# Kernel optimization log

Hardware: AMD Instinct MI355X
Metric: run time of the kernel (lower is better)

The kernel has to match this reference:

```python
import jax, jax.numpy as jnp
import numpy as np

EMBED_DIM = 1024
NUM_HEADS = 16
HEAD_DIM = EMBED_DIM // NUM_HEADS
SCALING = HEAD_DIM ** -0.5
T, B = 1024, 4


def setup_inputs() -> dict:
    key = jax.random.key(0)
    k1, k2, k3, k4 = jax.random.split(key, 4)
    x_TBC = jax.random.normal(k1, (T, B, EMBED_DIM), dtype=jnp.float32)
    key_padding_mask = jnp.zeros((B, T), dtype=bool)
    edge_bias = jax.random.normal(k2, (B, NUM_HEADS, T, T), dtype=jnp.float32)
    # xavier_uniform-ish init for weights
    lim_qkv = (6.0 / (EMBED_DIM + 3 * EMBED_DIM)) ** 0.5 / (2 ** 0.5)
    w_qkv = jax.random.uniform(k3, (3 * EMBED_DIM, EMBED_DIM), minval=-lim_qkv, maxval=lim_qkv, dtype=jnp.float32)
    b_qkv = jnp.zeros((3 * EMBED_DIM,), dtype=jnp.float32)
    lim_p = (6.0 / (2 * EMBED_DIM)) ** 0.5
    w_proj = jax.random.uniform(k4, (EMBED_DIM, EMBED_DIM), minval=-lim_p, maxval=lim_p, dtype=jnp.float32)
    b_proj = jnp.zeros((EMBED_DIM,), dtype=jnp.float32)
    return {"x_TBC": x_TBC, "key_padding_mask": key_padding_mask, "edge_bias": edge_bias,
            "w_qkv": w_qkv, "b_qkv": b_qkv, "w_proj": w_proj, "b_proj": b_proj}


def reference(x_TBC, key_padding_mask, edge_bias, w_qkv, b_qkv, w_proj, b_proj):
    Tn, Bn, C = x_TBC.shape
    H, Dh = NUM_HEADS, HEAD_DIM
    qkv = x_TBC @ w_qkv.T + b_qkv               # [T,B,3C]
    q, k, v = jnp.split(qkv, 3, axis=-1)
    def split_heads(t):  # [T,B,C] -> [B,H,T,Dh]
        return t.reshape(Tn, Bn, H, Dh).transpose(1, 2, 0, 3)
    q = split_heads(q) * SCALING
    k = split_heads(k)
    v = split_heads(v)
    logits = jnp.einsum('bhtd,bhsd->bhts', q, k) + edge_bias  # [B,H,T,T]
    neg_inf = jnp.finfo(logits.dtype).min
    logits = jnp.where(key_padding_mask[:, None, None, :], neg_inf, logits)
    attn = jax.nn.softmax(logits, axis=-1)
    out = jnp.einsum('bhts,bhsd->bhtd', attn, v)  # [B,H,T,Dh]
    out = out.transpose(2, 0, 1, 3).reshape(Tn, Bn, C)  # [T,B,C]
    out = out @ w_proj.T + b_proj
    return out
```

## Files before the change

kernel.cpp:

```cpp
#include <hip/hip_runtime.h>
#include <stdint.h>
#include <math.h>

#define TT  1024
#define BBN 4
#define CCH 1024
#define HHN 16
#define DHD 64
#define MMR 4096
#define N3  3072

typedef __attribute__((ext_vector_type(4))) float  f32x4;
typedef __attribute__((ext_vector_type(8))) short  s16x8;
typedef __attribute__((ext_vector_type(8))) __bf16 bf16x8;

static __device__ __forceinline__ f32x4 mfma16(s16x8 a, s16x8 b, f32x4 c) {
  return __builtin_amdgcn_mfma_f32_16x16x32_bf16(
      __builtin_bit_cast(bf16x8, a), __builtin_bit_cast(bf16x8, b), c, 0, 0, 0);
}

static __device__ __forceinline__ unsigned short f2bf(float f) {
  union { float f; unsigned int u; } v; v.f = f;
  unsigned int u = v.u;
  return (unsigned short)((u + 0x7FFFu + ((u >> 16) & 1u)) >> 16);
}

typedef const __attribute__((address_space(1))) void GVoid;
typedef __attribute__((address_space(3))) void LVoid;
static __device__ __forceinline__ void gll16(const void* g, void* l) {
  __builtin_amdgcn_global_load_lds((GVoid*)g, (LVoid*)l, 16, 0, 0);
}

#if __has_builtin(__builtin_amdgcn_exp2f)
#define EXP2F(x) __builtin_amdgcn_exp2f(x)
#else
#define EXP2F(x) exp2f(x)
#endif

__global__ void cvt_all(const float* __restrict__ x, const float* __restrict__ wqkv,
                        const float* __restrict__ wproj, unsigned short* __restrict__ out) {
  int i = blockIdx.x * blockDim.x + threadIdx.x;
  const float4* src;
  int off;
  if (i < 1048576)      { src = (const float4*)x;     off = 0; }
  else if (i < 1835008) { src = (const float4*)wqkv;  off = 1048576; }
  else                  { src = (const float4*)wproj; off = 1835008; }
  float4 f = src[i - off];
  ushort4 o;
  o.x = f2bf(f.x); o.y = f2bf(f.y); o.z = f2bf(f.z); o.w = f2bf(f.w);
  ((ushort4*)out)[i] = o;
}

__global__ __launch_bounds__(512, 2) void gemm_qkv(
    const unsigned short* __restrict__ A, const unsigned short* __restrict__ Bw,
    const float* __restrict__ bias,
    unsigned short* __restrict__ qb, unsigned short* __restrict__ kb,
    unsigned short* __restrict__ vtb) {
  constexpr int K = 1024;
  constexpr int AH = 256 * 32;
  constexpr int BH = 256 * 32;
  __shared__ __align__(16) unsigned short sMem[3 * AH + 3 * BH];
  unsigned short* sA0 = sMem;
  unsigned short* sB0 = sMem + 3 * AH;
  const int tid = threadIdx.x;
  const int l = tid & 63, w = tid >> 6;
  const int g = l >> 4, c = l & 15;
  const int wr = w >> 2, wc = w & 3;
  const int total = gridDim.x * gridDim.y;
  const int flat = blockIdx.y * gridDim.x + blockIdx.x;
  const int wg = (flat & 7) * (total >> 3) + (flat >> 3);
  const int bxs = wg % gridDim.x, bys = wg / gridDim.x;
  const int bm = bys * 256, bn = bxs * 256;

  const int srow = tid >> 2;
  const int schG = (tid & 3) ^ ((tid >> 3) & 3);
  const unsigned short* Agp = A + (size_t)(bm + srow) * K + schG * 8;
  const unsigned short* Bgp = Bw + (size_t)(bn + srow) * K + schG * 8;
  const int swzR = (c >> 1) & 3;

  f32x4 acc[8][4] = {};

#define QSTAGE(s, h) do {                                                        \
    _Pragma("unroll")                                                            \
    for (int i_ = 0; i_ < 2; ++i_)                                               \
      gll16(Agp + (size_t)(i_ * 128) * K + (s) * 32,                             \
            sA0 + (h) * AH + i_ * 4096 + w * 512);                               \
    _Pragma("unroll")                                                            \
    for (int i_ = 0; i_ < 2; ++i_)                                               \
      gll16(Bgp + (size_t)(i_ * 128) * K + (s) * 32,                             \
            sB0 + (h) * BH + i_ * 4096 + w * 512);                               \
  } while (0)

  const int NS = K >> 5;
  QSTAGE(0, 0);
  QSTAGE(1, 1);
  QSTAGE(2, 2);
  asm volatile("s_waitcnt vmcnt(8)" ::: "memory");
  __builtin_amdgcn_s_barrier();

  int h = 0;
#pragma unroll 1
  for (int s = 0;; ++s) {
    s16x8 af[8], bfr[4];
#pragma unroll
    for (int mi = 0; mi < 8; ++mi)
      af[mi] = *(const s16x8*)&sA0[h * AH + (wr * 128 + mi * 16 + c) * 32 + (g ^ swzR) * 8];
#pragma unroll
    for (int ni = 0; ni < 4; ++ni)
      bfr[ni] = *(const s16x8*)&sB0[h * BH + (wc * 64 + ni * 16 + c) * 32 + (g ^ swzR) * 8];
#pragma unroll
    for (int mi = 0; mi < 8; ++mi)
#pragma unroll
      for (int ni = 0; ni < 4; ++ni)
        acc[mi][ni] = mfma16(af[mi], bfr[ni], acc[mi][ni]);
    if (s == NS - 1) break;
    __builtin_amdgcn_s_barrier();
    if (s + 3 < NS)      { QSTAGE(s + 3, h);
                           asm volatile("s_waitcnt vmcnt(8)" ::: "memory"); }
    else if (s + 2 < NS) { asm volatile("s_waitcnt vmcnt(4)" ::: "memory"); }
    else                 { asm volatile("s_waitcnt vmcnt(0)" ::: "memory"); }
    __builtin_amdgcn_s_barrier();
    h = (h == 2) ? 0 : h + 1;
  }

#undef QSTAGE

  const int part = bn >> 10;
  if (part != 2) {
    const bool isq = (part == 0);
    const float qscale = 0.18033688f;
#pragma unroll
    for (int mi = 0; mi < 8; ++mi)
#pragma unroll
      for (int ni = 0; ni < 4; ++ni) {
        const int col = bn + wc * 64 + ni * 16 + c;
        const float bsv = bias[col];
        const int rem = col & 1023;
        const int hh = rem >> 6, d = rem & 63;
#pragma unroll
        for (int j = 0; j < 4; ++j) {
          const int r = bm + wr * 128 + mi * 16 + g * 4 + j;
          const int t = r >> 2, bb = r & 3;
          const int bh = bb * 16 + hh;
          float av = acc[mi][ni][j] + bsv;
          if (isq) qb[((size_t)bh * 1024 + t) * 64 + d] = f2bf(av * qscale);
          else     kb[((size_t)bh * 1024 + t) * 64 + d] = f2bf(av);
        }
      }
    return;
  }

  unsigned short* sT = sMem;
  const int tl0 = bm >> 2;
  const int bb = w & 3, th = w >> 2;
#pragma unroll 1
  for (int pc = 0; pc < 4; ++pc) {
    __syncthreads();
    if (wc == pc) {
#pragma unroll
      for (int mi = 0; mi < 8; ++mi)
#pragma unroll
        for (int ni = 0; ni < 4; ++ni) {
          const int col = bn + pc * 64 + ni * 16 + c;
          const float bsv = bias[col];
#pragma unroll
          for (int j = 0; j < 4; ++j)
            sT[(wr * 128 + mi * 16 + g * 4 + j) * 72 + ni * 16 + c] =
                f2bf(acc[mi][ni][j] + bsv);
        }
    }
    __syncthreads();
    const int h2 = ((bn + pc * 64) & 1023) >> 6;
    unsigned short* vdst = vtb + ((size_t)(bb * 16 + h2) * 64 + l) * 1024 + tl0 + th * 32;
#pragma unroll
    for (int q8 = 0; q8 < 4; ++q8) {
      unsigned short pk[8];
#pragma unroll
      for (int e = 0; e < 8; ++e)
        pk[e] = sT[(((th * 32 + q8 * 8 + e) << 2) | bb) * 72 + l];
      *(s16x8*)&vdst[q8 * 8] = *(const s16x8*)pk;
    }
  }
}

template <int MODE, int BN>
__global__ __launch_bounds__(256, 4) void gemm_bt(
    const unsigned short* __restrict__ A, const unsigned short* __restrict__ Bw,
    const float* __restrict__ bias, float* __restrict__ Cout, int M, int N, int K) {
  constexpr int NI = BN / 32;
  constexpr int AH = 128 * 32;
  constexpr int BH = BN * 32;
  __shared__ __align__(16) unsigned short sMem[3 * AH + 3 * BH];
  unsigned short* sA0 = sMem;
  unsigned short* sB0 = sMem + 3 * AH;
  const int tid = threadIdx.x;
  const int l = tid & 63, w = tid >> 6;
  const int g = l >> 4, c = l & 15;
  const int wr = w >> 1, wc = w & 1;
  const int total = gridDim.x * gridDim.y;
  const int flat = blockIdx.y * gridDim.x + blockIdx.x;
  const int wg = (flat & 7) * (total >> 3) + (flat >> 3);
  const int bxs = wg % gridDim.x, bys = wg / gridDim.x;
  const int bm = bys * 128, bn = bxs * BN;

  const int srow = w * 16 + (l >> 2);
  const int schG = (l & 3) ^ ((l >> 3) & 3);
  const unsigned short* Agp = A + (size_t)(bm + srow) * K + schG * 8;
  const unsigned short* Bgp = Bw + (size_t)(bn + srow) * K + schG * 8;
  const int swzR = (c >> 1) & 3;

  f32x4 acc[4][NI] = {};

#define GSTAGE(s, h) do {                                                        \
    _Pragma("unroll")                                                            \
    for (int i_ = 0; i_ < 2; ++i_)                                               \
      gll16(Agp + (size_t)(i_ * 64) * K + (s) * 32,                              \
            sA0 + (h) * AH + i_ * 2048 + w * 512);                               \
    _Pragma("unroll")                                                            \
    for (int i_ = 0; i_ < BN / 64; ++i_)                                         \
      gll16(Bgp + (size_t)(i_ * 64) * K + (s) * 32,                              \
            sB0 + (h) * BH + i_ * 2048 + w * 512);                               \
  } while (0)

  const int NS = K >> 5;
  GSTAGE(0, 0);
  GSTAGE(1, 1);
  GSTAGE(2, 2);
  asm volatile("s_waitcnt vmcnt(6)" ::: "memory");
  __builtin_amdgcn_s_barrier();

  int h = 0;
#pragma unroll 1
  for (int s = 0;; ++s) {
    s16x8 af[4], bfr[NI];
#pragma unroll
    for (int mi = 0; mi < 4; ++mi)
      af[mi] = *(const s16x8*)&sA0[h * AH + (wr * 64 + mi * 16 + c) * 32 + (g ^ swzR) * 8];
#pragma unroll
    for (int ni = 0; ni < NI; ++ni)
      bfr[ni] = *(const s16x8*)&sB0[h * BH + (wc * (BN / 2) + ni * 16 + c) * 32 + (g ^ swzR) * 8];
#pragma unroll
    for (int mi = 0; mi < 4; ++mi)
#pragma unroll
      for (int ni = 0; ni < NI; ++ni)
        acc[mi][ni] = mfma16(af[mi], bfr[ni], acc[mi][ni]);
    if (s == NS - 1) break;
    __builtin_amdgcn_s_barrier();
    if (s + 3 < NS)      { GSTAGE(s + 3, h);
                           asm volatile("s_waitcnt vmcnt(6)" ::: "memory"); }
    else if (s + 2 < NS) { asm volatile("s_waitcnt vmcnt(3)" ::: "memory"); }
    else                 { asm volatile("s_waitcnt vmcnt(0)" ::: "memory"); }
    __builtin_amdgcn_s_barrier();
    h = (h == 2) ? 0 : h + 1;
  }

#undef GSTAGE

#pragma unroll
  for (int mi = 0; mi < 4; ++mi)
#pragma unroll
    for (int ni = 0; ni < NI; ++ni) {
      const int col = bn + wc * (BN / 2) + ni * 16 + c;
      const float bsv = bias[col];
#pragma unroll
      for (int j = 0; j < 4; ++j) {
        const int r = bm + wr * 64 + mi * 16 + g * 4 + j;
        Cout[(size_t)r * N + col] = acc[mi][ni][j] + bsv;
      }
    }
}

__global__ __launch_bounds__(256, 3) void attn_kernel(
    const unsigned short* __restrict__ qb, const unsigned short* __restrict__ kb,
    const unsigned short* __restrict__ vtb, const float* __restrict__ eb,
    const unsigned char* __restrict__ mask, unsigned short* __restrict__ ob) {
  __shared__ __align__(16) unsigned short sQ[64 * 64];
  __shared__ __align__(16) unsigned short sK[2][64 * 64];
  __shared__ __align__(16) unsigned short sV[2][64 * 64];
  __shared__ __align__(16) unsigned short sP[4][16 * 72];
  __shared__ __align__(4) unsigned char sM[1024];
  const int tid = threadIdx.x;
  const int l = tid & 63, w = tid >> 6;
  const int g = l >> 4, c = l & 15;
  const int flat = blockIdx.y * 16 + blockIdx.x;
  const int wg = (flat & 7) * 128 + (flat >> 3);
  const int q0 = (wg & 15) * 64;
  const int bh = wg >> 4;
  const int b = bh >> 4;
  const int srow = tid >> 3, sch = tid & 7;

  const unsigned short* qg = qb + (size_t)bh * 65536;
  const unsigned short* kg = kb + (size_t)bh * 65536;
  const unsigned short* vg = vtb + (size_t)bh * 65536;
  const float* ebg = eb + (size_t)bh * 1048576 + (size_t)(q0 + w * 16 + g * 4) * 1024;

  const float BS = 1.44269504f;
  float bvA[4][4], bvB[4][4];
  float ps[4] = {0.f, 0.f, 0.f, 0.f};
  f32x4 po[4] = {};

#define STAGE(tv, P) do {                                                        \
    _Pragma("unroll")                                                            \
    for (int i_ = 0; i_ < 2; ++i_) {                                             \
      int row_ = i_ * 32 + srow;                                                 \
      gll16(kg + (size_t)((tv) * 64 + row_) * 64 + (sch ^ (row_ & 7)) * 8,       \
            &sK[P][i_ * 2048 + w * 512]);                                        \
      gll16(vg + (size_t)row_ * 1024 + (tv) * 64 + (sch ^ (row_ & 7)) * 8,       \
            &sV[P][i_ * 2048 + w * 512]);                                        \
    } } while (0)

#define BIAS(tv, BV) do {                                                        \
    _Pragma("unroll")                                                            \
    for (int ni_ = 0; ni_ < 4; ++ni_)                                            \
      _Pragma("unroll")                                                          \
      for (int j_ = 0; j_ < 4; ++j_)                                             \
        BV[ni_][j_] = ebg[(size_t)j_ * 1024 + (tv) * 64 + ni_ * 16 + c];         \
    } while (0)

#define TILE(P, BV, s0v) do {                                                    \
    float mkc_[4];                                                               \
    _Pragma("unroll")                                                            \
    for (int ni_ = 0; ni_ < 4; ++ni_)                                            \
      mkc_[ni_] = sM[(s0v) + ni_ * 16 + c] ? -1e30f : -8.0f;                     \
    s16x8 kf_[4][2];                                                             \
    _Pragma("unroll")                                                            \
    for (int ni_ = 0; ni_ < 4; ++ni_)                                            \
      _Pragma("unroll")                                                          \
      for (int k2_ = 0; k2_ < 2; ++k2_) {                                        \
        int row_ = ni_ * 16 + c;                                                 \
        kf_[ni_][k2_] = *(const s16x8*)&sK[P][row_ * 64 +                        \
                         (((k2_ * 4 + g) ^ (row_ & 7)) * 8)];                    \
      }                                                                          \
    f32x4 sc_[4] = {};                                                           \
    _Pragma("unroll")                                                            \
    for (int k2_ = 0; k2_ < 2; ++k2_)                                            \
      _Pragma("unroll")                                                          \
      for (int ni_ = 0; ni_ < 4; ++ni_)                                          \
        sc_[ni_] = mfma16(qf[k2_], kf_[ni_][k2_], sc_[ni_]);                     \
    _Pragma("unroll")                                                            \
    for (int ni_ = 0; ni_ < 4; ++ni_)                                            \
      _Pragma("unroll")                                                          \
      for (int j_ = 0; j_ < 4; ++j_) {                                           \
        float x_ = fmaf(BV[ni_][j_], BS, sc_[ni_][j_]) + mkc_[ni_];              \
        float p_ = EXP2F(x_);                                                    \
        sP[w][(g * 4 + j_) * 72 + ni_ * 16 + c] = f2bf(p_);                      \
        ps[j_] += p_;                                                            \
      }                                                                          \
    s16x8 vf_[4][2];                                                             \
    _Pragma("unroll")                                                            \
    for (int nd_ = 0; nd_ < 4; ++nd_)                                            \
      _Pragma("unroll")                                                          \
      for (int k2_ = 0; k2_ < 2; ++k2_) {                                        \
        int row_ = nd_ * 16 + c;                                                 \
        vf_[nd_][k2_] = *(const s16x8*)&sV[P][row_ * 64 +                        \
                         (((k2_ * 4 + g) ^ (row_ & 7)) * 8)];                    \
      }                                                                          \
    asm volatile("s_waitcnt lgkmcnt(0)" ::: "memory");                           \
    __builtin_amdgcn_sched_barrier(0);                                           \
    s16x8 pf_[2];                                                                \
    _Pragma("unroll")                                                            \
    for (int k2_ = 0; k2_ < 2; ++k2_)                                            \
      pf_[k2_] = *(const s16x8*)&sP[w][c * 72 + k2_ * 32 + g * 8];               \
    _Pragma("unroll")                                                            \
    for (int k2_ = 0; k2_ < 2; ++k2_)                                            \
      _Pragma("unroll")                                                          \
      for (int nd_ = 0; nd_ < 4; ++nd_)                                          \
        po[nd_] = mfma16(pf_[k2_], vf_[nd_][k2_], po[nd_]);                      \
  } while (0)

#pragma unroll
  for (int i = 0; i < 2; ++i) {
    int row = i * 32 + srow;
    gll16(qg + (size_t)(q0 + row) * 64 + (sch ^ (row & 7)) * 8, &sQ[i * 2048 + w * 512]);
  }
  STAGE(0, 0);
  STAGE(1, 1);
  BIAS(0, bvA);
  BIAS(1, bvB);
  ((unsigned int*)sM)[tid] = ((const unsigned int*)(mask + b * TT))[tid & 255];
  __syncthreads();

  s16x8 qf[2];
#pragma unroll
  for (int kk2 = 0; kk2 < 2; ++kk2) {
    int row = w * 16 + c;
    qf[kk2] = *(const s16x8*)&sQ[row * 64 + (((kk2 * 4 + g) ^ (row & 7)) * 8)];
  }

#pragma unroll 1
  for (int t2 = 0;; t2 += 2) {
    TILE(0, bvA, t2 * 64);
    __builtin_amdgcn_s_barrier();
    if (t2 + 2 < 16) { STAGE(t2 + 2, 0); BIAS(t2 + 2, bvA); }
    if (t2 == 14) { asm volatile("s_waitcnt vmcnt(16)" ::: "memory"); }
    else          { asm volatile("s_waitcnt vmcnt(36)" ::: "memory"); }
    __builtin_amdgcn_s_barrier();
    TILE(1, bvB, t2 * 64 + 64);
    if (t2 == 14) break;
    __builtin_amdgcn_s_barrier();
    STAGE(t2 + 3, 1); BIAS(t2 + 3, bvB);
    asm volatile("s_waitcnt vmcnt(36)" ::: "memory");
    __builtin_amdgcn_s_barrier();
  }

#undef STAGE
#undef BIAS
#undef TILE

#pragma unroll
  for (int j = 0; j < 4; ++j) {
#pragma unroll
    for (int off = 1; off <= 8; off <<= 1)
      ps[j] += __shfl_xor(ps[j], off, 64);
    ps[j] = 1.0f / ps[j];
  }
  const int h = bh & 15;
#pragma unroll
  for (int nd = 0; nd < 4; ++nd)
#pragma unroll
    for (int j = 0; j < 4; ++j) {
      float val = po[nd][j] * ps[j];
      int t = q0 + w * 16 + g * 4 + j;
      ob[((size_t)t * 4 + b) * 1024 + h * 64 + nd * 16 + c] = f2bf(val);
    }
}

extern "C" void kernel_launch(void* const* d_in, const int* in_sizes, int n_in,
                              void* d_out, int out_size, void* d_ws, size_t ws_size,
                              hipStream_t stream) {
  const float* x      = (const float*)d_in[0];
  const unsigned char* mask = (const unsigned char*)d_in[1];
  const float* ebias  = (const float*)d_in[2];
  const float* wqkv   = (const float*)d_in[3];
  const float* bqkv   = (const float*)d_in[4];
  const float* wproj  = (const float*)d_in[5];
  const float* bproj  = (const float*)d_in[6];
  float* out = (float*)d_out;

  char* ws = (char*)d_ws;
  unsigned short* xb    = (unsigned short*)(ws);
  unsigned short* wqkvb = (unsigned short*)(ws + 8388608);
  unsigned short* wpb   = (unsigned short*)(ws + 14680064);
  unsigned short* qbuf  = (unsigned short*)(ws + 16777216);
  unsigned short* kbuf  = (unsigned short*)(ws + 25165824);
  unsigned short* vtbuf = (unsigned short*)(ws + 33554432);
  unsigned short* obuf  = (unsigned short*)(ws + 41943040);

  cvt_all<<<8192, 256, 0, stream>>>(x, wqkv, wproj, xb);

  gemm_qkv<<<dim3(12, 16), 512, 0, stream>>>(
      xb, wqkvb, bqkv, qbuf, kbuf, vtbuf);

  attn_kernel<<<dim3(16, 64), 256, 0, stream>>>(
      qbuf, kbuf, vtbuf, ebias, mask, obuf);

  gemm_bt<0, 64><<<dim3(16, 32), 256, 0, stream>>>(
      obuf, wpb, bproj, out, MMR, 1024, 1024);
}
```

Before: 157.5 us.

## Restructure QKV GEMM main loop into interleaved load/MFMA double-buffered pipeline

Replaces the 3-stage 32-wide K pipeline in the QKV projection GEMM with a 2-tile-deep scheme of 64-wide K tiles split into halves, using 4 LDS planes per operand. Global-to-LDS loads for the next tile are issued between LDS fragment reads and MFMA groups, and s_setprio raises wave priority around the MFMA bursts. The A fragments are read in halves to cut register pressure, and explicit lgkmcnt waits with sched_barriers fix the ordering. LDS use grows from 6 to 8 planes, which may affect the two-blocks-per-CU occupancy target.

```diff
diff --git a/kernel.cpp b/kernel.cpp
--- a/kernel.cpp
+++ b/kernel.cpp
@@ -57,11 +57,10 @@
     unsigned short* __restrict__ qb, unsigned short* __restrict__ kb,
     unsigned short* __restrict__ vtb) {
   constexpr int K = 1024;
-  constexpr int AH = 256 * 32;
-  constexpr int BH = 256 * 32;
-  __shared__ __align__(16) unsigned short sMem[3 * AH + 3 * BH];
+  constexpr int PH = 256 * 32;
+  __shared__ __align__(16) unsigned short sMem[8 * PH];
   unsigned short* sA0 = sMem;
-  unsigned short* sB0 = sMem + 3 * AH;
+  unsigned short* sB0 = sMem + 4 * PH;
   const int tid = threadIdx.x;
   const int l = tid & 63, w = tid >> 6;
   const int g = l >> 4, c = l & 15;
@@ -80,50 +79,60 @@
 
   f32x4 acc[8][4] = {};
 
-#define QSTAGE(s, h) do {                                                        \
-    _Pragma("unroll")                                                            \
-    for (int i_ = 0; i_ < 2; ++i_)                                               \
-      gll16(Agp + (size_t)(i_ * 128) * K + (s) * 32,                             \
-            sA0 + (h) * AH + i_ * 4096 + w * 512);                               \
-    _Pragma("unroll")                                                            \
-    for (int i_ = 0; i_ < 2; ++i_)                                               \
-      gll16(Bgp + (size_t)(i_ * 128) * K + (s) * 32,                             \
-            sB0 + (h) * BH + i_ * 4096 + w * 512);                               \
+#define QST(tt, rh, kh2) do {                                                    \
+    const int po_ = (((((tt) & 1) << 1) | (kh2)) * PH) + (rh) * 4096 + w * 512;  \
+    gll16(Agp + (size_t)((rh) * 128) * K + (tt) * 64 + (kh2) * 32, sA0 + po_);   \
+    gll16(Bgp + (size_t)((rh) * 128) * K + (tt) * 64 + (kh2) * 32, sB0 + po_);   \
   } while (0)
-
-  const int NS = K >> 5;
-  QSTAGE(0, 0);
-  QSTAGE(1, 1);
-  QSTAGE(2, 2);
-  asm volatile("s_waitcnt vmcnt(8)" ::: "memory");
-  __builtin_amdgcn_s_barrier();
-
-  int h = 0;
+#define RD_B(pl) do { _Pragma("unroll")                                          \
+    for (int ni = 0; ni < 4; ++ni)                                               \
+      bfr[ni] = *(const s16x8*)&sB0[(pl) * PH + (wc * 64 + ni * 16 + c) * 32 +   \
+                                    (g ^ swzR) * 8]; } while (0)
+#define RD_A(pl, mh) do { _Pragma("unroll")                                      \
+    for (int q = 0; q < 4; ++q)                                                  \
+      af[q] = *(const s16x8*)&sA0[(pl) * PH +                                    \
+               (wr * 128 + ((mh) * 4 + q) * 16 + c) * 32 + (g ^ swzR) * 8]; } while (0)
+#define MM(mh) do {                                                              \
+    __builtin_amdgcn_s_setprio(1);                                               \
+    _Pragma("unroll")                                                            \
+    for (int q = 0; q < 4; ++q)                                                  \
+      _Pragma("unroll")                                                          \
+      for (int ni = 0; ni < 4; ++ni)                                             \
+        acc[(mh) * 4 + q][ni] = mfma16(af[q], bfr[ni], acc[(mh) * 4 + q][ni]);   \
+    __builtin_amdgcn_s_setprio(0); } while (0)
+#define LKW do { asm volatile("s_waitcnt lgkmcnt(0)" ::: "memory");              \
+    __builtin_amdgcn_sched_barrier(0); } while (0)
+
+  QST(0, 0, 0); QST(0, 1, 0); QST(0, 0, 1); QST(0, 1, 1);
+
 #pragma unroll 1
-  for (int s = 0;; ++s) {
-    s16x8 af[8], bfr[4];
-#pragma unroll
-    for (int mi = 0; mi < 8; ++mi)
-      af[mi] = *(const s16x8*)&sA0[h * AH + (wr * 128 + mi * 16 + c) * 32 + (g ^ swzR) * 8];
-#pragma unroll
-    for (int ni = 0; ni < 4; ++ni)
-      bfr[ni] = *(const s16x8*)&sB0[h * BH + (wc * 64 + ni * 16 + c) * 32 + (g ^ swzR) * 8];
-#pragma unroll
-    for (int mi = 0; mi < 8; ++mi)
-#pragma unroll
-      for (int ni = 0; ni < 4; ++ni)
-        acc[mi][ni] = mfma16(af[mi], bfr[ni], acc[mi][ni]);
-    if (s == NS - 1) break;
-    __builtin_amdgcn_s_barrier();
-    if (s + 3 < NS)      { QSTAGE(s + 3, h);
-                           asm volatile("s_waitcnt vmcnt(8)" ::: "memory"); }
-    else if (s + 2 < NS) { asm volatile("s_waitcnt vmcnt(4)" ::: "memory"); }
-    else                 { asm volatile("s_waitcnt vmcnt(0)" ::: "memory"); }
-    __builtin_amdgcn_s_barrier();
-    h = (h == 2) ? 0 : h + 1;
-  }
-
-#undef QSTAGE
+  for (int t = 0; t < 16; ++t) {
+    const int pl0 = (t & 1) << 1, pl1 = pl0 + 1;
+    s16x8 af[4], bfr[4];
+    asm volatile("s_waitcnt vmcnt(4)" ::: "memory");
+    __builtin_amdgcn_s_barrier();
+    RD_B(pl0); RD_A(pl0, 0);
+    if (t < 15) QST(t + 1, 0, 0);
+    LKW; MM(0);
+    RD_A(pl0, 1);
+    if (t < 15) QST(t + 1, 1, 0);
+    LKW; MM(1);
+    if (t == 15) { asm volatile("s_waitcnt vmcnt(0)" ::: "memory"); }
+    else         { asm volatile("s_waitcnt vmcnt(4)" ::: "memory"); }
+    __builtin_amdgcn_s_barrier();
+    RD_B(pl1); RD_A(pl1, 0);
+    if (t < 15) QST(t + 1, 0, 1);
+    LKW; MM(0);
+    RD_A(pl1, 1);
+    if (t < 15) QST(t + 1, 1, 1);
+    LKW; MM(1);
+  }
+
+#undef QST
+#undef RD_B
+#undef RD_A
+#undef MM
+#undef LKW
 
   const int part = bn >> 10;
   if (part != 2) {
```

Result: faster. 151.5 us (-3.8%).
